# Kernel tuning notes

Measured on AMD Instinct MI355X. Metric: run time of the kernel, lower is better.

The kernel has to match this reference:

```python
import jax, jax.numpy as jnp
import numpy as np

B, S, H, NH = 2, 2048, 1024, 16
HD = H // NH  # 64


def setup_inputs() -> dict:
    key = jax.random.key(0)
    ks = jax.random.split(key, 9)
    w = lambda k: jax.random.normal(k, (H, H), dtype=jnp.float32) * 0.02  # torch Linear weight [out,in]
    b = lambda k: jax.random.normal(k, (H,), dtype=jnp.float32) * 0.02
    return {
        "hidden_states": jax.random.normal(ks[0], (B, S, H), dtype=jnp.float32),
        "Wq": w(ks[1]), "bq": b(ks[2]),
        "Wk": w(ks[3]), "bk": b(ks[4]),
        "Wv": w(ks[5]), "bv": b(ks[6]),
        "Wo": w(ks[7]), "bo": b(ks[8]),
    }


def reference(hidden_states, Wq, bq, Wk, bk, Wv, bv, Wo, bo):
    b, s, h = hidden_states.shape
    nh, hd = NH, h // NH

    def proj(W, bias):
        y = hidden_states @ W.T + bias  # torch Linear: x W^T + b
        return y.reshape(b, s, nh, hd).transpose(0, 2, 1, 3)  # [b, h, s, d]

    q = proj(Wq, bq)
    k = proj(Wk, bk)
    v = proj(Wv, bv)

    scale = jnp.sqrt(jnp.asarray(hd, dtype=q.dtype))
    scores = jnp.einsum("bhqd,bhkd->bhqk", q, k) / scale  # [b, h, s, s]
    pos = jnp.arange(s)
    causal = pos[:, None] < pos[None, :]  # True where masked (key after query)
    scores = jnp.where(causal[None, None], -jnp.inf, scores)
    attn = jax.nn.softmax(scores, axis=-1)
    out = jnp.einsum("bhqk,bhkd->bhqd", attn, v)
    out = out.transpose(0, 2, 1, 3).reshape(b, s, h)
    return out @ Wo.T + bo
```

## Files before the change

kernel.cpp:

```cpp
#include <hip/hip_runtime.h>
#include <stdint.h>

typedef __bf16 bf16;
typedef __attribute__((ext_vector_type(2))) __bf16 bf16x2;
typedef __attribute__((ext_vector_type(4))) __bf16 bf16x4;
typedef __attribute__((ext_vector_type(8))) __bf16 bf16x8;
typedef __attribute__((ext_vector_type(4))) float f32x4;
typedef __attribute__((ext_vector_type(4))) short s16x4;

#define B_  2
#define S_  2048
#define H_  1024
#define NH_ 16
#define HD_ 64

__device__ __forceinline__ void glds16(const bf16* g, bf16* l) {
  __builtin_amdgcn_global_load_lds(
      (const __attribute__((address_space(1))) uint32_t*)g,
      (__attribute__((address_space(3))) uint32_t*)l, 16, 0, 0);
}

__device__ __forceinline__ f32x4 pv_mfma(bf16x4 a, bf16x4 b, f32x4 c) {
#if __has_builtin(__builtin_amdgcn_mfma_f32_16x16x16bf16_1k)
  union U { bf16x4 h; s16x4 s; };
  U ua; ua.h = a;
  U ub; ub.h = b;
  return __builtin_amdgcn_mfma_f32_16x16x16bf16_1k(ua.s, ub.s, c, 0, 0, 0);
#else
  f32x4 d;
  asm volatile("v_mfma_f32_16x16x16_bf16 %0, %1, %2, %3\n\ts_nop 7\n\ts_nop 7"
               : "=v"(d) : "v"(a), "v"(b), "v"(c));
  return d;
#endif
}

__global__ __launch_bounds__(256) void cvt_f32_bf16(
    const float* __restrict__ s0, bf16* __restrict__ d0, int n0,
    const float* __restrict__ s1, bf16* __restrict__ d1,
    const float* __restrict__ s2, bf16* __restrict__ d2,
    const float* __restrict__ s3, bf16* __restrict__ d3,
    const float* __restrict__ s4, bf16* __restrict__ d4, int nw)
{
  const float* s; bf16* d; int n;
  switch (blockIdx.y) {
    case 0:  s = s0; d = d0; n = n0; break;
    case 1:  s = s1; d = d1; n = nw; break;
    case 2:  s = s2; d = d2; n = nw; break;
    case 3:  s = s3; d = d3; n = nw; break;
    default: s = s4; d = d4; n = nw; break;
  }
  const int i = (blockIdx.x * 256 + threadIdx.x) * 8;
  if (i >= n) return;
  float4 v0 = *(const float4*)(s + i);
  float4 v1 = *(const float4*)(s + i + 4);
  bf16x8 o;
  o[0] = (bf16)v0.x; o[1] = (bf16)v0.y; o[2] = (bf16)v0.z; o[3] = (bf16)v0.w;
  o[4] = (bf16)v1.x; o[5] = (bf16)v1.y; o[6] = (bf16)v1.z; o[7] = (bf16)v1.w;
  *(bf16x8*)(d + i) = o;
}

__global__ __launch_bounds__(512, 2) void gemm_qkv_8ph(
    const bf16* __restrict__ X,
    const bf16* __restrict__ Wc,
    const float* __restrict__ bq, const float* __restrict__ bk,
    const float* __restrict__ bv,
    bf16* __restrict__ Yq, bf16* __restrict__ Yk, bf16* __restrict__ Yv,
    float qscl)
{
  constexpr int K  = 1024;
  constexpr int NT = K / 64;

  __shared__ __align__(16) bf16 As[2][256 * 64];
  __shared__ __align__(16) bf16 Bs[2][256 * 64];

  const int f   = blockIdx.x;
  const int swz = (f & 7) * 24 + (f >> 3);
  const int by  = swz / 12, bx = swz % 12;
  const int m0  = by * 256, n0 = bx * 256;

  const int tid  = threadIdx.x;
  const int lane = tid & 63;
  const int wave = tid >> 6;
  const int quad = lane >> 4;
  const int l15  = lane & 15;
  const int wm   = (wave >> 2) * 128;
  const int wn   = (wave & 3) * 64;

  const int r0  = tid >> 3;
  const int kc0 = tid & 7;

  const bf16* Xb = X  + (size_t)m0 * K;
  const bf16* Wb = Wc + (size_t)n0 * K;

  f32x4 acc[8][4] = {};

#define SBAR() asm volatile("s_barrier" ::: "memory")
#define VM0()  asm volatile("s_waitcnt vmcnt(0)" ::: "memory")
#define STG(MAT, G, cb_, h)                                                 \
  { _Pragma("unroll") for (int s = 0; s < 2; ++s) {                         \
      const int row = (h) * 128 + s * 64 + r0;                              \
      const int sc  = kc0 ^ (row & 7);                                      \
      glds16((G) + (size_t)row * K + sc * 8,                                \
             &MAT[cb_][((h) * 1024 + s * 512 + wave * 64) * 8]); } }
#define RA(mi, ks) (*(const bf16x8*)&As[cb][(wm + (mi) * 16 + l15) * 64 +   \
                     ((((ks) * 4 + quad)) ^ (l15 & 7)) * 8])
#define RB(ni, ks) (*(const bf16x8*)&Bs[cb][(wn + (ni) * 16 + l15) * 64 +   \
                     ((((ks) * 4 + quad)) ^ (l15 & 7)) * 8])
#define MFMA(d, x, y) d = __builtin_amdgcn_mfma_f32_16x16x32_bf16(x, y, d, 0, 0, 0)

  STG(As, Xb, 0, 0); STG(As, Xb, 0, 1);
  STG(Bs, Wb, 0, 0); STG(Bs, Wb, 0, 1);
  VM0();
  SBAR();

  for (int t = 0; t < NT; ++t) {
    const int cb = t & 1, sb = cb ^ 1;
    const bf16* Xn = Xb + (t + 1) * 64;
    const bf16* Wn = Wb + (t + 1) * 64;
    const bool pre = (t + 1 < NT);

    bf16x8 a[4][2], b[4][2];

#pragma unroll
    for (int mi = 0; mi < 4; ++mi) { a[mi][0] = RA(mi, 0); a[mi][1] = RA(mi, 1); }
#pragma unroll
    for (int ni = 0; ni < 2; ++ni) { b[ni][0] = RB(ni, 0); b[ni][1] = RB(ni, 1); }
    if (pre) { STG(As, Xn, sb, 0); STG(As, Xn, sb, 1); }
    SBAR();
    __builtin_amdgcn_s_setprio(1);
#pragma unroll
    for (int mi = 0; mi < 4; ++mi)
#pragma unroll
      for (int ni = 0; ni < 2; ++ni) {
        MFMA(acc[mi][ni], a[mi][0], b[ni][0]);
        MFMA(acc[mi][ni], a[mi][1], b[ni][1]);
      }
    __builtin_amdgcn_s_setprio(0);
    SBAR();

#pragma unroll
    for (int ni = 2; ni < 4; ++ni) { b[ni][0] = RB(ni, 0); b[ni][1] = RB(ni, 1); }
    if (pre) { STG(Bs, Wn, sb, 0); STG(Bs, Wn, sb, 1); }
    SBAR();
    __builtin_amdgcn_s_setprio(1);
#pragma unroll
    for (int mi = 0; mi < 4; ++mi)
#pragma unroll
      for (int ni = 2; ni < 4; ++ni) {
        MFMA(acc[mi][ni], a[mi][0], b[ni][0]);
        MFMA(acc[mi][ni], a[mi][1], b[ni][1]);
      }
    __builtin_amdgcn_s_setprio(0);
    SBAR();

#pragma unroll
    for (int mi = 0; mi < 4; ++mi) { a[mi][0] = RA(mi + 4, 0); a[mi][1] = RA(mi + 4, 1); }
    SBAR();
    __builtin_amdgcn_s_setprio(1);
#pragma unroll
    for (int mi = 0; mi < 4; ++mi)
#pragma unroll
      for (int ni = 0; ni < 2; ++ni) {
        MFMA(acc[mi + 4][ni], a[mi][0], b[ni][0]);
        MFMA(acc[mi + 4][ni], a[mi][1], b[ni][1]);
      }
    __builtin_amdgcn_s_setprio(0);
    SBAR();

    __builtin_amdgcn_s_setprio(1);
#pragma unroll
    for (int mi = 0; mi < 4; ++mi)
#pragma unroll
      for (int ni = 2; ni < 4; ++ni) {
        MFMA(acc[mi + 4][ni], a[mi][0], b[ni][0]);
        MFMA(acc[mi + 4][ni], a[mi][1], b[ni][1]);
      }
    __builtin_amdgcn_s_setprio(0);
    VM0();
    SBAR();
  }

  const int seg = bx >> 2;
  const float* bias = seg == 0 ? bq : (seg == 1 ? bk : bv);
  bf16* Yp = seg == 0 ? Yq : (seg == 1 ? Yk : Yv);
  const float ysc = seg == 0 ? qscl : 1.0f;
  const int nc0 = n0 - seg * 1024;
#pragma unroll
  for (int mi = 0; mi < 8; ++mi) {
    const int row = m0 + wm + mi * 16 + quad * 4;
#pragma unroll
    for (int ni = 0; ni < 4; ++ni) {
      const int col = nc0 + wn + ni * 16 + l15;
      const float bvv = bias[col];
#pragma unroll
      for (int r = 0; r < 4; ++r)
        Yp[(size_t)(row + r) * H_ + col] = (bf16)((acc[mi][ni][r] + bvv) * ysc);
    }
  }
#undef SBAR
#undef VM0
#undef STG
#undef RA
#undef RB
#undef MFMA
}

template <typename TY>
__global__ __launch_bounds__(256) void gemm_bt_bias(
    const bf16* __restrict__ X, const bf16* __restrict__ W,
    const float* __restrict__ bias, TY* __restrict__ Y,
    int M, int N, int K)
{
  __shared__ __align__(16) bf16 As[2][128 * 32];
  __shared__ __align__(16) bf16 Bs[2][128 * 32];

  const int tid  = threadIdx.x;
  const int lane = tid & 63;
  const int wave = tid >> 6;
  const int m0 = blockIdx.y * 128;
  const int n0 = blockIdx.x * 128;
  const int wm = (wave >> 1) * 64;
  const int wn = (wave & 1) * 64;

  const int r0 = tid >> 2,            c0 = (tid & 3) * 8;
  const int r1 = (256 + tid) >> 2,    c1 = ((256 + tid) & 3) * 8;
  const int cb0 = (wave * 64) * 8;
  const int cb1 = (256 + wave * 64) * 8;

  f32x4 acc[4][4] = {};

  glds16(X + (size_t)(m0 + r0) * K + c0, &As[0][cb0]);
  glds16(W + (size_t)(n0 + r0) * K + c0, &Bs[0][cb0]);
  glds16(X + (size_t)(m0 + r1) * K + c1, &As[0][cb1]);
  glds16(W + (size_t)(n0 + r1) * K + c1, &Bs[0][cb1]);

  int pb = 0;
  for (int k0 = 0; k0 < K; k0 += 32, pb ^= 1) {
    __syncthreads();

    if (k0 + 32 < K) {
      const int kn = k0 + 32;
      glds16(X + (size_t)(m0 + r0) * K + kn + c0, &As[pb ^ 1][cb0]);
      glds16(W + (size_t)(n0 + r0) * K + kn + c0, &Bs[pb ^ 1][cb0]);
      glds16(X + (size_t)(m0 + r1) * K + kn + c1, &As[pb ^ 1][cb1]);
      glds16(W + (size_t)(n0 + r1) * K + kn + c1, &Bs[pb ^ 1][cb1]);
    }

    bf16x8 a[4], b[4];
#pragma unroll
    for (int i = 0; i < 4; ++i)
      a[i] = *(const bf16x8*)&As[pb][(wm + i * 16 + (lane & 15)) * 32 + (lane >> 4) * 8];
#pragma unroll
    for (int i = 0; i < 4; ++i)
      b[i] = *(const bf16x8*)&Bs[pb][(wn + i * 16 + (lane & 15)) * 32 + (lane >> 4) * 8];
#pragma unroll
    for (int mi = 0; mi < 4; ++mi)
#pragma unroll
      for (int ni = 0; ni < 4; ++ni)
        acc[mi][ni] = __builtin_amdgcn_mfma_f32_16x16x32_bf16(a[mi], b[ni], acc[mi][ni], 0, 0, 0);
  }

#pragma unroll
  for (int mi = 0; mi < 4; ++mi) {
    const int row = m0 + wm + mi * 16 + (lane >> 4) * 4;
#pragma unroll
    for (int ni = 0; ni < 4; ++ni) {
      const int col = n0 + wn + ni * 16 + (lane & 15);
      const float bv = bias[col];
#pragma unroll
      for (int r = 0; r < 4; ++r)
        Y[(size_t)(row + r) * N + col] = (TY)(acc[mi][ni][r] + bv);
    }
  }
}

__device__ __forceinline__ void attn_tile_step(
    const bf16* Ksb, const bf16* Vtb, const bf16x8 bq[2], int qrow, int k0,
    bool maskit, float& mr, float& lr, f32x4 oacc[4], int l15, int quad)
{
  f32x4 sacc[8] = {};
  __builtin_amdgcn_s_setprio(1);
#pragma unroll
  for (int ks = 0; ks < 2; ++ks) {
#pragma unroll
    for (int mb = 0; mb < 8; ++mb) {
      const int row = mb * 16 + l15;
      const int ch  = (ks * 4 + quad) ^ (l15 & 7);
      bf16x8 ak = *(const bf16x8*)&Ksb[row * 64 + ch * 8];
      sacc[mb] = __builtin_amdgcn_mfma_f32_16x16x32_bf16(ak, bq[ks], sacc[mb], 0, 0, 0);
    }
  }
  __builtin_amdgcn_s_setprio(0);

  if (maskit) {
#pragma unroll
    for (int mb = 0; mb < 8; ++mb) {
      const int kb = k0 + mb * 16 + quad * 4;
#pragma unroll
      for (int r = 0; r < 4; ++r)
        if (kb + r > qrow) sacc[mb][r] = -1e30f;
    }
  }

  float mx = -1e30f;
#pragma unroll
  for (int mb = 0; mb < 8; ++mb)
    mx = fmaxf(mx, fmaxf(fmaxf(sacc[mb][0], sacc[mb][1]),
                         fmaxf(sacc[mb][2], sacc[mb][3])));
  mx = fmaxf(mx, __shfl_xor(mx, 16, 64));
  mx = fmaxf(mx, __shfl_xor(mx, 32, 64));

  float sum = 0.0f;
  bf16x4 pwv[8];
#pragma unroll
  for (int mb = 0; mb < 8; ++mb) {
    bf16x4 pw;
#pragma unroll
    for (int r = 0; r < 4; ++r) {
      const float p = __builtin_amdgcn_exp2f(sacc[mb][r] - mr);
      sum += p;
      pw[r] = (bf16)p;
    }
    pwv[mb] = pw;
  }
  sum += __shfl_xor(sum, 16, 64);
  sum += __shfl_xor(sum, 32, 64);

  __builtin_amdgcn_s_setprio(1);
#pragma unroll
  for (int mb = 0; mb < 8; ++mb) {
#pragma unroll
    for (int db = 0; db < 4; ++db) {
      const int vch = (mb * 4 + quad) ^ ((l15 & 7) << 2) ^ ((l15 >> 3) & 1) ^ (db << 1);
      bf16x4 av = *(const bf16x4*)&Vtb[(db * 16 + l15) * 128 + vch * 4];
      oacc[db] = pv_mfma(av, pwv[mb], oacc[db]);
    }
  }
  __builtin_amdgcn_s_setprio(0);

  lr += sum;
  if (!__all(mx <= mr + 8.0f)) {
    const float mnew  = fmaxf(mr, mx);
    const float alpha = __builtin_amdgcn_exp2f(mr - mnew);
    lr *= alpha;
#pragma unroll
    for (int db = 0; db < 4; ++db)
#pragma unroll
      for (int r = 0; r < 4; ++r) oacc[db][r] *= alpha;
    mr = mnew;
  }
}

__global__ __launch_bounds__(512, 4) void attn_causal(
    const bf16* __restrict__ Q, const bf16* __restrict__ K,
    const bf16* __restrict__ V, bf16* __restrict__ O)
{
  const int lin  = blockIdx.x;
  const int slot = lin >> 3;
  const int bh   = (lin & 7) * 4 + (slot >> 4);
  const int pair = slot & 15;
  const int b    = bh >> 4;
  const int h    = bh & 15;

  const int tid  = threadIdx.x;
  const int lane = tid & 63;
  const int wave = tid >> 6;
  const int quad = lane >> 4;
  const int l15  = lane & 15;
  const size_t headoff = (size_t)b * S_ * H_ + (size_t)h * HD_;
  const bf16* Kp = K + headoff;
  const bf16* Vp = V + headoff;

  __shared__ __align__(16) bf16 Ks[2][128 * 64];
  __shared__ __align__(16) bf16 Vt[2][64 * 128];

  const int qlo = pair, qhi = 31 - pair;
  const int nl  = (qlo >> 1) + 1;
  const int nh  = (qhi >> 1) + 1;
  const bool isH = wave < 4;
  const int  myq = isH ? qhi : qlo;
  const int  myn = isH ? nh  : nl;
  const int qrow = myq * 64 + (wave & 3) * 16 + l15;

  bf16x8 bq[2];
  bq[0] = *(const bf16x8*)(Q + headoff + (size_t)qrow * H_ + quad * 8);
  bq[1] = *(const bf16x8*)(Q + headoff + (size_t)qrow * H_ + 32 + quad * 8);

  const int kp = tid & 63;
  const int g  = tid >> 6;

#define STAGE_K(k0_, buf_)                                                  \
  {                                                                         \
    _Pragma("unroll")                                                       \
    for (int i = 0; i < 2; ++i) {                                           \
      const int n = i * 512 + tid;                                          \
      const int row = n >> 3;                                               \
      const int cg  = (n & 7) ^ (row & 7);                                  \
      glds16(Kp + (size_t)((k0_) + row) * H_ + cg * 8,                      \
             &Ks[buf_][(i * 512 + wave * 64) * 8]);                         \
    }                                                                       \
  }

#define LOAD_V(k0_)                                                         \
  {                                                                         \
    vreg[0] = *(const bf16x8*)(Vp + (size_t)((k0_) + 2 * kp) * H_ + g * 8); \
    vreg[1] = *(const bf16x8*)(Vp + (size_t)((k0_) + 2 * kp + 1) * H_ + g * 8);\
  }

#define WRITE_V(buf_)                                                       \
  {                                                                         \
    _Pragma("unroll")                                                       \
    for (int e = 0; e < 8; ++e) {                                           \
      const int row = g * 8 + e;                                            \
      const int pos = (kp >> 1) ^ ((row & 7) << 2) ^ ((row >> 3) & 1)       \
                      ^ ((row >> 4) << 1);                                  \
      bf16x2 pw; pw[0] = vreg[0][e]; pw[1] = vreg[1][e];                    \
      *(bf16x2*)&Vt[buf_][row * 128 + pos * 4 + ((2 * kp) & 3)] = pw;       \
    }                                                                       \
  }

  bf16x8 vreg[2];

  STAGE_K(0, 0);
  LOAD_V(0);
  WRITE_V(0);
  __syncthreads();

  float mr = 0.0f, lr = 0.0f;
  f32x4 oacc[4] = {};

  for (int it = 0; it < nh; ++it) {
    const int c = it & 1;
    const bool pre = (it + 1 < nh);

    if (pre) {
      STAGE_K((it + 1) * 128, c ^ 1);
      LOAD_V((it + 1) * 128);
    }

    if (it < myn)
      attn_tile_step(Ks[c], Vt[c], bq, qrow, it * 128, it == myn - 1,
                     mr, lr, oacc, l15, quad);

    if (pre) {
      WRITE_V(c ^ 1);
      __syncthreads();
    }
  }

  const float inv = 1.0f / lr;
#pragma unroll
  for (int db = 0; db < 4; ++db) {
    bf16x4 o;
#pragma unroll
    for (int r = 0; r < 4; ++r) o[r] = (bf16)(oacc[db][r] * inv);
    *(bf16x4*)(O + headoff + (size_t)qrow * H_ + db * 16 + quad * 4) = o;
  }
#undef STAGE_K
#undef LOAD_V
#undef WRITE_V
}

extern "C" void kernel_launch(void* const* d_in, const int* in_sizes, int n_in,
                              void* d_out, int out_size, void* d_ws, size_t ws_size,
                              hipStream_t stream) {
  const float* hs = (const float*)d_in[0];
  const float* Wq = (const float*)d_in[1]; const float* bq = (const float*)d_in[2];
  const float* Wk = (const float*)d_in[3]; const float* bk = (const float*)d_in[4];
  const float* Wv = (const float*)d_in[5]; const float* bv = (const float*)d_in[6];
  const float* Wo = (const float*)d_in[7]; const float* bo = (const float*)d_in[8];
  float* out = (float*)d_out;

  const size_t elems = (size_t)B_ * S_ * H_;
  const size_t wel   = (size_t)H_ * H_;
  bf16* hsb = (bf16*)d_ws;
  bf16* AO  = hsb;
  bf16* Wqb = hsb + elems;
  bf16* Wkb = Wqb + wel;
  bf16* Wvb = Wkb + wel;
  bf16* Wob = Wvb + wel;
  bf16* Qw  = Wob + wel;
  bf16* Kw  = Qw + elems;
  bf16* Vw  = Kw + elems;

  cvt_f32_bf16<<<dim3(2048, 5), dim3(256), 0, stream>>>(
      hs, hsb, (int)elems, Wq, Wqb, Wk, Wkb, Wv, Wvb, Wo, Wob, (int)wel);

  const int M = B_ * S_;
  const float QSCL = 0.125f * 1.44269504f;

  gemm_qkv_8ph<<<dim3(192), dim3(512), 0, stream>>>(
      hsb, Wqb, bq, bk, bv, Qw, Kw, Vw, QSCL);

  attn_causal<<<dim3(512), dim3(512), 0, stream>>>(Qw, Kw, Vw, AO);

  gemm_bt_bias<float><<<dim3(H_ / 128, M / 128), dim3(256), 0, stream>>>(
      AO, Wob, bo, out, M, H_, H_);
}
```

Baseline: 204.5 us.

## Process low and high query tiles per wave to share K/V LDS reads

Each wave now owns both the low and the high causal query tile, where previously half the waves took each. Every K and V fragment loaded from LDS feeds two MFMAs instead of one, and the block shrinks to 256 threads, so K/V staging is spread over more iterations per thread. To keep the order of the two matrix phases, the online-softmax rescale now also scales the pending bf16 probabilities before the PV product. The trade-off is roughly double the accumulator and Q register footprint per wave, plus branches on the low tile that may limit occupancy.

```diff
diff --git a/kernel.cpp b/kernel.cpp
--- a/kernel.cpp
+++ b/kernel.cpp
@@ -274,24 +274,10 @@
   }
 }
 
-__device__ __forceinline__ void attn_tile_step(
-    const bf16* Ksb, const bf16* Vtb, const bf16x8 bq[2], int qrow, int k0,
-    bool maskit, float& mr, float& lr, f32x4 oacc[4], int l15, int quad)
+__device__ __forceinline__ void softmax_pv_half(
+    f32x4 sacc[8], const bf16* Vtb, int qrow, int k0, bool maskit,
+    float& mr, float& lr, f32x4 oacc[4], bf16x4 pwv[8], int l15, int quad)
 {
-  f32x4 sacc[8] = {};
-  __builtin_amdgcn_s_setprio(1);
-#pragma unroll
-  for (int ks = 0; ks < 2; ++ks) {
-#pragma unroll
-    for (int mb = 0; mb < 8; ++mb) {
-      const int row = mb * 16 + l15;
-      const int ch  = (ks * 4 + quad) ^ (l15 & 7);
-      bf16x8 ak = *(const bf16x8*)&Ksb[row * 64 + ch * 8];
-      sacc[mb] = __builtin_amdgcn_mfma_f32_16x16x32_bf16(ak, bq[ks], sacc[mb], 0, 0, 0);
-    }
-  }
-  __builtin_amdgcn_s_setprio(0);
-
   if (maskit) {
 #pragma unroll
     for (int mb = 0; mb < 8; ++mb) {
@@ -311,7 +297,6 @@
   mx = fmaxf(mx, __shfl_xor(mx, 32, 64));
 
   float sum = 0.0f;
-  bf16x4 pwv[8];
 #pragma unroll
   for (int mb = 0; mb < 8; ++mb) {
     bf16x4 pw;
@@ -325,20 +310,8 @@
   }
   sum += __shfl_xor(sum, 16, 64);
   sum += __shfl_xor(sum, 32, 64);
-
-  __builtin_amdgcn_s_setprio(1);
-#pragma unroll
-  for (int mb = 0; mb < 8; ++mb) {
-#pragma unroll
-    for (int db = 0; db < 4; ++db) {
-      const int vch = (mb * 4 + quad) ^ ((l15 & 7) << 2) ^ ((l15 >> 3) & 1) ^ (db << 1);
-      bf16x4 av = *(const bf16x4*)&Vtb[(db * 16 + l15) * 128 + vch * 4];
-      oacc[db] = pv_mfma(av, pwv[mb], oacc[db]);
-    }
-  }
-  __builtin_amdgcn_s_setprio(0);
-
   lr += sum;
+
   if (!__all(mx <= mr + 8.0f)) {
     const float mnew  = fmaxf(mr, mx);
     const float alpha = __builtin_amdgcn_exp2f(mr - mnew);
@@ -347,11 +320,18 @@
     for (int db = 0; db < 4; ++db)
 #pragma unroll
       for (int r = 0; r < 4; ++r) oacc[db][r] *= alpha;
+#pragma unroll
+    for (int mb = 0; mb < 8; ++mb) {
+      bf16x4 pw = pwv[mb];
+#pragma unroll
+      for (int r = 0; r < 4; ++r) pw[r] = (bf16)((float)pw[r] * alpha);
+      pwv[mb] = pw;
+    }
     mr = mnew;
   }
 }
 
-__global__ __launch_bounds__(512, 4) void attn_causal(
+__global__ __launch_bounds__(256, 2) void attn_causal(
     const bf16* __restrict__ Q, const bf16* __restrict__ K,
     const bf16* __restrict__ V, bf16* __restrict__ O)
 {
@@ -377,14 +357,14 @@
   const int qlo = pair, qhi = 31 - pair;
   const int nl  = (qlo >> 1) + 1;
   const int nh  = (qhi >> 1) + 1;
-  const bool isH = wave < 4;
-  const int  myq = isH ? qhi : qlo;
-  const int  myn = isH ? nh  : nl;
-  const int qrow = myq * 64 + (wave & 3) * 16 + l15;
-
-  bf16x8 bq[2];
-  bq[0] = *(const bf16x8*)(Q + headoff + (size_t)qrow * H_ + quad * 8);
-  bq[1] = *(const bf16x8*)(Q + headoff + (size_t)qrow * H_ + 32 + quad * 8);
+  const int qrowL = qlo * 64 + wave * 16 + l15;
+  const int qrowH = qhi * 64 + wave * 16 + l15;
+
+  bf16x8 bqL[2], bqH[2];
+  bqL[0] = *(const bf16x8*)(Q + headoff + (size_t)qrowL * H_ + quad * 8);
+  bqL[1] = *(const bf16x8*)(Q + headoff + (size_t)qrowL * H_ + 32 + quad * 8);
+  bqH[0] = *(const bf16x8*)(Q + headoff + (size_t)qrowH * H_ + quad * 8);
+  bqH[1] = *(const bf16x8*)(Q + headoff + (size_t)qrowH * H_ + 32 + quad * 8);
 
   const int kp = tid & 63;
   const int g  = tid >> 6;
@@ -392,55 +372,91 @@
 #define STAGE_K(k0_, buf_)                                                  \
   {                                                                         \
     _Pragma("unroll")                                                       \
-    for (int i = 0; i < 2; ++i) {                                           \
-      const int n = i * 512 + tid;                                          \
+    for (int i = 0; i < 4; ++i) {                                           \
+      const int n = i * 256 + tid;                                          \
       const int row = n >> 3;                                               \
       const int cg  = (n & 7) ^ (row & 7);                                  \
       glds16(Kp + (size_t)((k0_) + row) * H_ + cg * 8,                      \
-             &Ks[buf_][(i * 512 + wave * 64) * 8]);                         \
+             &Ks[buf_][(i * 256 + wave * 64) * 8]);                         \
     }                                                                       \
   }
 
 #define LOAD_V(k0_)                                                         \
   {                                                                         \
-    vreg[0] = *(const bf16x8*)(Vp + (size_t)((k0_) + 2 * kp) * H_ + g * 8); \
-    vreg[1] = *(const bf16x8*)(Vp + (size_t)((k0_) + 2 * kp + 1) * H_ + g * 8);\
+    vreg[0] = *(const bf16x8*)(Vp + (size_t)((k0_) + 2 * kp) * H_ + g * 16);     \
+    vreg[1] = *(const bf16x8*)(Vp + (size_t)((k0_) + 2 * kp) * H_ + g * 16 + 8); \
+    vreg[2] = *(const bf16x8*)(Vp + (size_t)((k0_) + 2 * kp + 1) * H_ + g * 16);     \
+    vreg[3] = *(const bf16x8*)(Vp + (size_t)((k0_) + 2 * kp + 1) * H_ + g * 16 + 8); \
   }
 
 #define WRITE_V(buf_)                                                       \
   {                                                                         \
     _Pragma("unroll")                                                       \
-    for (int e = 0; e < 8; ++e) {                                           \
-      const int row = g * 8 + e;                                            \
+    for (int e = 0; e < 16; ++e) {                                          \
+      const int row = g * 16 + e;                                           \
       const int pos = (kp >> 1) ^ ((row & 7) << 2) ^ ((row >> 3) & 1)       \
                       ^ ((row >> 4) << 1);                                  \
-      bf16x2 pw; pw[0] = vreg[0][e]; pw[1] = vreg[1][e];                    \
-      *(bf16x2*)&Vt[buf_][row * 128 + pos * 4 + ((2 * kp) & 3)] = pw;       \
+      bf16x2 pw;                                                            \
+      pw[0] = (e < 8) ? vreg[0][e & 7] : vreg[1][e & 7];                    \
+      pw[1] = (e < 8) ? vreg[2][e & 7] : vreg[3][e & 7];                    \
+      *(bf16x2*)&Vt[buf_][row * 128 + pos * 4 + (kp & 1) * 2] = pw;         \
     }                                                                       \
   }
 
-  bf16x8 vreg[2];
+  bf16x8 vreg[4];
 
   STAGE_K(0, 0);
   LOAD_V(0);
   WRITE_V(0);
   __syncthreads();
 
-  float mr = 0.0f, lr = 0.0f;
-  f32x4 oacc[4] = {};
+  float mrL = 0.0f, lrL = 0.0f, mrH = 0.0f, lrH = 0.0f;
+  f32x4 oL[4] = {}, oH[4] = {};
 
   for (int it = 0; it < nh; ++it) {
     const int c = it & 1;
     const bool pre = (it + 1 < nh);
+    const bool doL = (it < nl);
+    const int k0 = it * 128;
 
     if (pre) {
       STAGE_K((it + 1) * 128, c ^ 1);
       LOAD_V((it + 1) * 128);
     }
 
-    if (it < myn)
-      attn_tile_step(Ks[c], Vt[c], bq, qrow, it * 128, it == myn - 1,
-                     mr, lr, oacc, l15, quad);
+    f32x4 sH[8] = {}, sL[8] = {};
+    __builtin_amdgcn_s_setprio(1);
+#pragma unroll
+    for (int ks = 0; ks < 2; ++ks) {
+#pragma unroll
+      for (int mb = 0; mb < 8; ++mb) {
+        const int row = mb * 16 + l15;
+        const int ch  = (ks * 4 + quad) ^ (l15 & 7);
+        bf16x8 ak = *(const bf16x8*)&Ks[c][row * 64 + ch * 8];
+        sH[mb] = __builtin_amdgcn_mfma_f32_16x16x32_bf16(ak, bqH[ks], sH[mb], 0, 0, 0);
+        if (doL)
+          sL[mb] = __builtin_amdgcn_mfma_f32_16x16x32_bf16(ak, bqL[ks], sL[mb], 0, 0, 0);
+      }
+    }
+    __builtin_amdgcn_s_setprio(0);
+
+    bf16x4 pwH[8], pwL[8];
+    softmax_pv_half(sH, Vt[c], qrowH, k0, it == nh - 1, mrH, lrH, oH, pwH, l15, quad);
+    if (doL)
+      softmax_pv_half(sL, Vt[c], qrowL, k0, it == nl - 1, mrL, lrL, oL, pwL, l15, quad);
+
+    __builtin_amdgcn_s_setprio(1);
+#pragma unroll
+    for (int mb = 0; mb < 8; ++mb) {
+#pragma unroll
+      for (int db = 0; db < 4; ++db) {
+        const int vch = (mb * 4 + quad) ^ ((l15 & 7) << 2) ^ ((l15 >> 3) & 1) ^ (db << 1);
+        bf16x4 av = *(const bf16x4*)&Vt[c][(db * 16 + l15) * 128 + vch * 4];
+        oH[db] = pv_mfma(av, pwH[mb], oH[db]);
+        if (doL) oL[db] = pv_mfma(av, pwL[mb], oL[db]);
+      }
+    }
+    __builtin_amdgcn_s_setprio(0);
 
     if (pre) {
       WRITE_V(c ^ 1);
@@ -448,13 +464,21 @@
     }
   }
 
-  const float inv = 1.0f / lr;
+  const float invH = 1.0f / lrH;
 #pragma unroll
   for (int db = 0; db < 4; ++db) {
     bf16x4 o;
 #pragma unroll
-    for (int r = 0; r < 4; ++r) o[r] = (bf16)(oacc[db][r] * inv);
-    *(bf16x4*)(O + headoff + (size_t)qrow * H_ + db * 16 + quad * 4) = o;
+    for (int r = 0; r < 4; ++r) o[r] = (bf16)(oH[db][r] * invH);
+    *(bf16x4*)(O + headoff + (size_t)qrowH * H_ + db * 16 + quad * 4) = o;
+  }
+  const float invL = 1.0f / lrL;
+#pragma unroll
+  for (int db = 0; db < 4; ++db) {
+    bf16x4 o;
+#pragma unroll
+    for (int r = 0; r < 4; ++r) o[r] = (bf16)(oL[db][r] * invL);
+    *(bf16x4*)(O + headoff + (size_t)qrowL * H_ + db * 16 + quad * 4) = o;
   }
 #undef STAGE_K
 #undef LOAD_V
@@ -492,7 +516,7 @@
   gemm_qkv_8ph<<<dim3(192), dim3(512), 0, stream>>>(
       hsb, Wqb, bq, bk, bv, Qw, Kw, Vw, QSCL);
 
-  attn_causal<<<dim3(512), dim3(512), 0, stream>>>(Qw, Kw, Vw, AO);
+  attn_causal<<<dim3(512), dim3(256), 0, stream>>>(Qw, Kw, Vw, AO);
 
   gemm_bt_bias<float><<<dim3(H_ / 128, M / 128), dim3(256), 0, stream>>>(
       AO, Wob, bo, out, M, H_, H_);
```

Measured after the change: 516.6 us. 2.53x slower.
